# Optimization experiments

Measured on AMD Instinct MI355X. Metric: run time of the kernel, lower is better.

The kernel has to match this reference:

```python
import jax, jax.numpy as jnp
import numpy as np

B, SECL, WORDL, DIM = 16, 16, 256, 1024  # src_len = SECL*WORDL = 4096, dim = 2*hidden_dim
F_SIZE = 2  # config.mode == 'train'


def setup_inputs() -> dict:
    key = jax.random.key(0)
    ks = jax.random.split(key, 10)
    S = SECL * WORDL
    return {
        "dec_hidden": jax.random.normal(ks[0], (B, DIM), jnp.float32),
        "enc_output": jax.random.normal(ks[1], (B, S, DIM), jnp.float32),
        "enc_feature": jax.random.normal(ks[2], (B, S, DIM), jnp.float32),
        "enc_mask": jnp.ones((B, S), jnp.float32),
        "sec_attn": jax.random.uniform(ks[3], (B, SECL), jnp.float32),
        "coverage": jax.random.uniform(ks[4], (B, S), jnp.float32),
        "focus": jax.random.normal(ks[5], (B, SECL), jnp.float32),
        "W_dec": jax.random.normal(ks[6], (DIM, DIM), jnp.float32) * 0.02,
        "b_dec": jax.random.normal(ks[7], (DIM,), jnp.float32) * 0.02,
        "v": jax.random.normal(ks[8], (DIM,), jnp.float32) * 0.02,
        "w_cov": jax.random.normal(ks[9], (DIM,), jnp.float32) * 0.02,
    }


def reference(dec_hidden, enc_output, enc_feature, enc_mask, sec_attn, coverage, focus,
              W_dec, b_dec, v, w_cov):
    batch, src_len, dim = enc_output.shape
    secL = sec_attn.shape[1]
    wordL = src_len // secL

    # decode_proj(dec_hidden), broadcast over src_len; coverage feature = coverage * w_cov
    dec_feature = dec_hidden @ W_dec.T + b_dec                     # [B, D]
    att_features = (enc_feature + dec_feature[:, None, :]
                    + coverage[:, :, None] * w_cov[None, None, :])  # [B, S, D]
    score = jnp.einsum('bsd,d->bs', jnp.tanh(att_features), v)      # [B, S]

    # hard focus path: top-k sections, gather scores/mask, softmax, scatter back
    score3 = score.reshape(batch, secL, wordL)
    topk_focus, top_idx = jax.lax.top_k(focus, F_SIZE)              # [B, k]
    bidx = jnp.arange(batch)[:, None]
    score_g = score3[bidx, top_idx].reshape(batch, -1)              # [B, k*wordL]
    mask_g = enc_mask.reshape(batch, secL, wordL)[bidx, top_idx].reshape(batch, -1)

    attn_foc = jax.nn.softmax(score_g, axis=1) * mask_g
    attn_foc = attn_foc / attn_foc.sum(1, keepdims=True)
    attn_foc = topk_focus[:, :, None] * attn_foc.reshape(batch, F_SIZE, wordL)

    attn_full = jnp.zeros((batch, secL, wordL), score.dtype).at[bidx, top_idx, :].set(attn_foc)
    attn_dist = attn_full.reshape(batch, src_len)
    attn_dist = attn_dist / attn_dist.sum(1, keepdims=True)

    context = jnp.einsum('bs,bsd->bd', attn_dist, enc_output)       # [B, D]
    coverage_out = coverage + attn_dist                              # [B, S]
    return context, attn_dist, coverage_out
```

## Files before the change

kernel.cpp:

```cpp
#include <hip/hip_runtime.h>
#include <math.h>

#define BB      16
#define SECL    16
#define WORDL   256
#define SRCLEN  4096
#define DIM     1024
#define FSZ     2
#define GL      (FSZ*WORDL)

__device__ __forceinline__ float fast_tanh(float x) {
    x = fminf(fmaxf(x, -10.f), 10.f);
    float e = __expf(2.f * x);
    return 1.f - 2.f * __builtin_amdgcn_rcpf(e + 1.f);
}

__global__ __launch_bounds__(256) void k_decproj_topk(
    const float* __restrict__ dec_hidden, const float* __restrict__ W_dec,
    const float* __restrict__ b_dec, const float* __restrict__ focus,
    float* __restrict__ dec_feature, int* __restrict__ top_idx,
    float* __restrict__ top_val, float* __restrict__ context)
{
    if (blockIdx.x == 16) {
        int b = blockIdx.y;
        float4 z = {0.f, 0.f, 0.f, 0.f};
        ((float4*)(context + (size_t)b * DIM))[threadIdx.x] = z;
        if (threadIdx.x == 0) {
            const float* f = focus + b * SECL;
            int i0 = 0; float v0 = f[0];
            for (int s = 1; s < SECL; s++) if (f[s] > v0) { v0 = f[s]; i0 = s; }
            int i1 = -1; float v1 = -INFINITY;
            for (int s = 0; s < SECL; s++)
                if (s != i0 && f[s] > v1) { v1 = f[s]; i1 = s; }
            top_idx[b*2+0] = i0; top_idx[b*2+1] = i1;
            top_val[b*2+0] = v0; top_val[b*2+1] = v1;
        }
        return;
    }
    int b = blockIdx.y;
    int t = threadIdx.x;
    int i = blockIdx.x * 64 + (t >> 2);
    int c = t & 3;
    const float4* Wr = (const float4*)(W_dec + (size_t)i * DIM + c * 256);
    const float4* Dr = (const float4*)(dec_hidden + (size_t)b * DIM + c * 256);
    float acc = 0.f;
    #pragma unroll 8
    for (int j = 0; j < 64; j++) {
        float4 w = Wr[j], d = Dr[j];
        acc += w.x*d.x + w.y*d.y + w.z*d.z + w.w*d.w;
    }
    acc += __shfl_down(acc, 2);
    acc += __shfl_down(acc, 1);
    if (c == 0) dec_feature[(size_t)b * DIM + i] = acc + b_dec[i];
}

__global__ __launch_bounds__(256) void k_score_cov(
    const float* __restrict__ enc_feature, const float* __restrict__ coverage,
    const float* __restrict__ dec_feature, const float* __restrict__ v,
    const float* __restrict__ w_cov, const int* __restrict__ top_idx,
    float* __restrict__ score_g, float* __restrict__ cov_out)
{
    int bid = blockIdx.x;
    if (bid >= 2048) {
        int idx = (bid - 2048) * 256 + threadIdx.x;
        ((float4*)cov_out)[idx] = ((const float4*)coverage)[idx];
        return;
    }
    int w    = bid * 4 + (threadIdx.x >> 6);
    int lane = threadIdx.x & 63;
    int b  = w >> 9;
    int r  = w & 511;
    int k  = r >> 8;
    int wp = r & 255;
    int sec = top_idx[b*2 + k];
    int s   = sec * WORDL + wp;
    float cv = coverage[(size_t)b * SRCLEN + s];
    const float4* ef = (const float4*)(enc_feature + ((size_t)b * SRCLEN + s) * DIM);
    const float4* df = (const float4*)(dec_feature + (size_t)b * DIM);
    const float4* vv = (const float4*)v;
    const float4* wc = (const float4*)w_cov;
    float acc = 0.f;
    #pragma unroll
    for (int q = 0; q < 4; q++) {
        int e4 = q * 64 + lane;
        float4 a = ef[e4], d = df[e4], wcv = wc[e4], vt = vv[e4];
        acc += fast_tanh(a.x + d.x + cv * wcv.x) * vt.x;
        acc += fast_tanh(a.y + d.y + cv * wcv.y) * vt.y;
        acc += fast_tanh(a.z + d.z + cv * wcv.z) * vt.z;
        acc += fast_tanh(a.w + d.w + cv * wcv.w) * vt.w;
    }
    #pragma unroll
    for (int off = 32; off; off >>= 1) acc += __shfl_down(acc, off);
    if (lane == 0) score_g[b * GL + r] = acc;
}

__device__ __forceinline__ float block_reduce(float val, int is_max) {
    __shared__ float red[4];
    int lane = threadIdx.x & 63, wid = threadIdx.x >> 6;
    #pragma unroll
    for (int off = 32; off; off >>= 1) {
        float o = __shfl_down(val, off);
        val = is_max ? fmaxf(val, o) : val + o;
    }
    if (lane == 0) red[wid] = val;
    __syncthreads();
    if (threadIdx.x == 0) {
        float r = red[0];
        for (int i = 1; i < 4; i++) r = is_max ? fmaxf(r, red[i]) : r + red[i];
        red[0] = r;
    }
    __syncthreads();
    float result = red[0];
    __syncthreads();
    return result;
}

__global__ __launch_bounds__(256) void k_softmax_scatter(
    const float* __restrict__ enc_mask, const float* __restrict__ coverage,
    const int* __restrict__ top_idx, const float* __restrict__ top_val,
    const float* __restrict__ score_g,
    float* __restrict__ attn_g, float* __restrict__ attn_out,
    float* __restrict__ cov_out)
{
    int b = blockIdx.x;
    int t = threadIdx.x;

    float4 z = {0.f, 0.f, 0.f, 0.f};
    float4* arow = (float4*)(attn_out + (size_t)b * SRCLEN);
    #pragma unroll
    for (int u = 0; u < 4; u++) arow[t + u * 256] = z;

    float sc[2], mk[2], fv[2];
    int ss[2];
    #pragma unroll
    for (int u = 0; u < 2; u++) {
        int r  = t + u * 256;
        int k  = r >> 8, wp = r & 255;
        int sec = top_idx[b*2 + k];
        int s   = sec * WORDL + wp;
        ss[u] = s;
        sc[u] = score_g[b * GL + r];
        mk[u] = enc_mask[(size_t)b * SRCLEN + s];
        fv[u] = top_val[b*2 + k];
    }
    float m  = block_reduce(fmaxf(sc[0], sc[1]), 1);
    float e0 = __expf(sc[0] - m), e1 = __expf(sc[1] - m);
    float Tn = block_reduce(fv[0]*e0*mk[0] + fv[1]*e1*mk[1], 0);
    float inv = 1.0f / Tn;
    __syncthreads();
    #pragma unroll
    for (int u = 0; u < 2; u++) {
        int r = t + u * 256;
        float a = fv[u] * (u ? e1 : e0) * mk[u] * inv;
        attn_g[b * GL + r] = a;
        attn_out[(size_t)b * SRCLEN + ss[u]] = a;
        cov_out [(size_t)b * SRCLEN + ss[u]] = coverage[(size_t)b * SRCLEN + ss[u]] + a;
    }
}

__global__ __launch_bounds__(256) void k_context(
    const float* __restrict__ enc_output, const int* __restrict__ top_idx,
    const float* __restrict__ attn_g, float* __restrict__ context)
{
    int b  = blockIdx.y;
    int sp = blockIdx.x;
    int t  = threadIdx.x;
    int i0 = top_idx[b*2], i1 = top_idx[b*2 + 1];
    float4 acc = {0.f, 0.f, 0.f, 0.f};
    #pragma unroll 4
    for (int j = 0; j < 32; j++) {
        int r  = sp * 32 + j;
        int k  = r >> 8, wp = r & 255;
        int s  = (k ? i1 : i0) * WORDL + wp;
        float a = attn_g[b * GL + r];
        float4 e = ((const float4*)(enc_output + ((size_t)b * SRCLEN + s) * DIM))[t];
        acc.x += a * e.x; acc.y += a * e.y; acc.z += a * e.z; acc.w += a * e.w;
    }
    float* ctx = context + (size_t)b * DIM + t * 4;
    atomicAdd(ctx + 0, acc.x);
    atomicAdd(ctx + 1, acc.y);
    atomicAdd(ctx + 2, acc.z);
    atomicAdd(ctx + 3, acc.w);
}

extern "C" void kernel_launch(void* const* d_in, const int* in_sizes, int n_in,
                              void* d_out, int out_size, void* d_ws, size_t ws_size,
                              hipStream_t stream) {
    const float* dec_hidden  = (const float*)d_in[0];
    const float* enc_output  = (const float*)d_in[1];
    const float* enc_feature = (const float*)d_in[2];
    const float* enc_mask    = (const float*)d_in[3];
    const float* coverage    = (const float*)d_in[5];
    const float* focus       = (const float*)d_in[6];
    const float* W_dec       = (const float*)d_in[7];
    const float* b_dec       = (const float*)d_in[8];
    const float* v           = (const float*)d_in[9];
    const float* w_cov       = (const float*)d_in[10];

    float* out      = (float*)d_out;
    float* context  = out;
    float* attn_out = out + 16384;
    float* cov_out  = out + 16384 + 65536;

    float* ws          = (float*)d_ws;
    float* dec_feature = ws;
    int*   top_idx     = (int*)(ws + 16384);
    float* top_val     = ws + 16384 + 32;
    float* score_g     = ws + 16448;
    float* attn_g      = ws + 24640;

    k_decproj_topk<<<dim3(17, 16), 256, 0, stream>>>(
        dec_hidden, W_dec, b_dec, focus, dec_feature, top_idx, top_val, context);

    k_score_cov<<<dim3(2112), 256, 0, stream>>>(
        enc_feature, coverage, dec_feature, v, w_cov, top_idx, score_g, cov_out);

    k_softmax_scatter<<<dim3(16), 256, 0, stream>>>(
        enc_mask, coverage, top_idx, top_val, score_g, attn_g, attn_out, cov_out);

    k_context<<<dim3(16, 16), 256, 0, stream>>>(
        enc_output, top_idx, attn_g, context);
}
```

Measured before the change: 458.4 us.

## Recompute top-2 per wave, fuse coverage update into context kernel, drop workspace

The serial single-thread top-2 over focus is replaced by a wave-level shuffle reduction. Each kernel recomputes it locally, so the top_idx and top_val buffers go away. The separate coverage copy plus scattered coverage writes become one vectorised coverage+attn pass in an extra block of the context kernel. That kernel now reads attention weights straight from attn_out. Intermediates (dec_feature, score_g) are aliased into output buffers instead of workspace, which relies on the kernel order to avoid overwriting live data.

```diff
diff --git a/kernel.cpp b/kernel.cpp
--- a/kernel.cpp
+++ b/kernel.cpp
@@ -9,32 +9,46 @@
 #define FSZ     2
 #define GL      (FSZ*WORDL)
 
+
 __device__ __forceinline__ float fast_tanh(float x) {
     x = fminf(fmaxf(x, -10.f), 10.f);
     float e = __expf(2.f * x);
     return 1.f - 2.f * __builtin_amdgcn_rcpf(e + 1.f);
 }
 
-__global__ __launch_bounds__(256) void k_decproj_topk(
+__device__ __forceinline__ void wave_top2(const float* __restrict__ f, int lane,
+                                          int& i0_, float& v0_, int& i1_, float& v1_)
+{
+    int idx = lane & 15;
+    float x = f[idx];
+    float m = x; int mi = idx;
+    #pragma unroll
+    for (int off = 8; off; off >>= 1) {
+        float om = __shfl_xor(m, off);
+        int   oi = __shfl_xor(mi, off);
+        if (om > m || (om == m && oi < mi)) { m = om; mi = oi; }
+    }
+    i0_ = mi; v0_ = m;
+    float x2 = (idx == mi) ? -INFINITY : x;
+    float m2 = x2; int mi2 = idx;
+    #pragma unroll
+    for (int off = 8; off; off >>= 1) {
+        float om = __shfl_xor(m2, off);
+        int   oi = __shfl_xor(mi2, off);
+        if (om > m2 || (om == m2 && oi < mi2)) { m2 = om; mi2 = oi; }
+    }
+    i1_ = mi2; v1_ = m2;
+}
+
+__global__ __launch_bounds__(256) void k_decproj(
     const float* __restrict__ dec_hidden, const float* __restrict__ W_dec,
-    const float* __restrict__ b_dec, const float* __restrict__ focus,
-    float* __restrict__ dec_feature, int* __restrict__ top_idx,
-    float* __restrict__ top_val, float* __restrict__ context)
+    const float* __restrict__ b_dec,
+    float* __restrict__ dec_feature, float* __restrict__ context)
 {
     if (blockIdx.x == 16) {
         int b = blockIdx.y;
         float4 z = {0.f, 0.f, 0.f, 0.f};
         ((float4*)(context + (size_t)b * DIM))[threadIdx.x] = z;
-        if (threadIdx.x == 0) {
-            const float* f = focus + b * SECL;
-            int i0 = 0; float v0 = f[0];
-            for (int s = 1; s < SECL; s++) if (f[s] > v0) { v0 = f[s]; i0 = s; }
-            int i1 = -1; float v1 = -INFINITY;
-            for (int s = 0; s < SECL; s++)
-                if (s != i0 && f[s] > v1) { v1 = f[s]; i1 = s; }
-            top_idx[b*2+0] = i0; top_idx[b*2+1] = i1;
-            top_val[b*2+0] = v0; top_val[b*2+1] = v1;
-        }
         return;
     }
     int b = blockIdx.y;
@@ -54,26 +68,24 @@
     if (c == 0) dec_feature[(size_t)b * DIM + i] = acc + b_dec[i];
 }
 
-__global__ __launch_bounds__(256) void k_score_cov(
+__global__ __launch_bounds__(256) void k_score(
     const float* __restrict__ enc_feature, const float* __restrict__ coverage,
     const float* __restrict__ dec_feature, const float* __restrict__ v,
-    const float* __restrict__ w_cov, const int* __restrict__ top_idx,
-    float* __restrict__ score_g, float* __restrict__ cov_out)
-{
-    int bid = blockIdx.x;
-    if (bid >= 2048) {
-        int idx = (bid - 2048) * 256 + threadIdx.x;
-        ((float4*)cov_out)[idx] = ((const float4*)coverage)[idx];
-        return;
-    }
-    int w    = bid * 4 + (threadIdx.x >> 6);
+    const float* __restrict__ w_cov, const float* __restrict__ focus,
+    float* __restrict__ score_g)
+{
+    int w    = blockIdx.x * 4 + (threadIdx.x >> 6);
     int lane = threadIdx.x & 63;
     int b  = w >> 9;
     int r  = w & 511;
     int k  = r >> 8;
     int wp = r & 255;
-    int sec = top_idx[b*2 + k];
+
+    int i0, i1; float v0, v1;
+    wave_top2(focus + b * SECL, lane, i0, v0, i1, v1);
+    int sec = k ? i1 : i0;
     int s   = sec * WORDL + wp;
+
     float cv = coverage[(size_t)b * SRCLEN + s];
     const float4* ef = (const float4*)(enc_feature + ((size_t)b * SRCLEN + s) * DIM);
     const float4* df = (const float4*)(dec_feature + (size_t)b * DIM);
@@ -116,14 +128,15 @@
 }
 
 __global__ __launch_bounds__(256) void k_softmax_scatter(
-    const float* __restrict__ enc_mask, const float* __restrict__ coverage,
-    const int* __restrict__ top_idx, const float* __restrict__ top_val,
-    const float* __restrict__ score_g,
-    float* __restrict__ attn_g, float* __restrict__ attn_out,
-    float* __restrict__ cov_out)
+    const float* __restrict__ enc_mask, const float* __restrict__ focus,
+    const float* __restrict__ score_g, float* __restrict__ attn_out)
 {
     int b = blockIdx.x;
     int t = threadIdx.x;
+    int lane = t & 63;
+
+    int i0, i1; float v0, v1;
+    wave_top2(focus + b * SECL, lane, i0, v0, i1, v1);
 
     float4 z = {0.f, 0.f, 0.f, 0.f};
     float4* arow = (float4*)(attn_out + (size_t)b * SRCLEN);
@@ -136,12 +149,12 @@
     for (int u = 0; u < 2; u++) {
         int r  = t + u * 256;
         int k  = r >> 8, wp = r & 255;
-        int sec = top_idx[b*2 + k];
+        int sec = k ? i1 : i0;
         int s   = sec * WORDL + wp;
         ss[u] = s;
         sc[u] = score_g[b * GL + r];
         mk[u] = enc_mask[(size_t)b * SRCLEN + s];
-        fv[u] = top_val[b*2 + k];
+        fv[u] = k ? v1 : v0;
     }
     float m  = block_reduce(fmaxf(sc[0], sc[1]), 1);
     float e0 = __expf(sc[0] - m), e1 = __expf(sc[1] - m);
@@ -152,27 +165,44 @@
     for (int u = 0; u < 2; u++) {
         int r = t + u * 256;
         float a = fv[u] * (u ? e1 : e0) * mk[u] * inv;
-        attn_g[b * GL + r] = a;
         attn_out[(size_t)b * SRCLEN + ss[u]] = a;
-        cov_out [(size_t)b * SRCLEN + ss[u]] = coverage[(size_t)b * SRCLEN + ss[u]] + a;
-    }
-}
-
-__global__ __launch_bounds__(256) void k_context(
-    const float* __restrict__ enc_output, const int* __restrict__ top_idx,
-    const float* __restrict__ attn_g, float* __restrict__ context)
+    }
+}
+
+__global__ __launch_bounds__(256) void k_context_cov(
+    const float* __restrict__ enc_output, const float* __restrict__ coverage,
+    const float* __restrict__ focus, const float* __restrict__ attn_out,
+    float* __restrict__ context, float* __restrict__ cov_out)
 {
     int b  = blockIdx.y;
     int sp = blockIdx.x;
     int t  = threadIdx.x;
-    int i0 = top_idx[b*2], i1 = top_idx[b*2 + 1];
+
+    if (sp == 16) {
+        const float4* cv = (const float4*)(coverage + (size_t)b * SRCLEN);
+        const float4* at = (const float4*)(attn_out + (size_t)b * SRCLEN);
+        float4*       co = (float4*)(cov_out + (size_t)b * SRCLEN);
+        #pragma unroll
+        for (int u = 0; u < 4; u++) {
+            int j = t + u * 256;
+            float4 c = cv[j], a = at[j];
+            c.x += a.x; c.y += a.y; c.z += a.z; c.w += a.w;
+            co[j] = c;
+        }
+        return;
+    }
+
+    int lane = t & 63;
+    int i0, i1; float v0, v1;
+    wave_top2(focus + b * SECL, lane, i0, v0, i1, v1);
+
     float4 acc = {0.f, 0.f, 0.f, 0.f};
     #pragma unroll 4
     for (int j = 0; j < 32; j++) {
         int r  = sp * 32 + j;
         int k  = r >> 8, wp = r & 255;
         int s  = (k ? i1 : i0) * WORDL + wp;
-        float a = attn_g[b * GL + r];
+        float a = attn_out[(size_t)b * SRCLEN + s];
         float4 e = ((const float4*)(enc_output + ((size_t)b * SRCLEN + s) * DIM))[t];
         acc.x += a * e.x; acc.y += a * e.y; acc.z += a * e.z; acc.w += a * e.w;
     }
@@ -202,22 +232,19 @@
     float* attn_out = out + 16384;
     float* cov_out  = out + 16384 + 65536;
 
-    float* ws          = (float*)d_ws;
-    float* dec_feature = ws;
-    int*   top_idx     = (int*)(ws + 16384);
-    float* top_val     = ws + 16384 + 32;
-    float* score_g     = ws + 16448;
-    float* attn_g      = ws + 24640;
-
-    k_decproj_topk<<<dim3(17, 16), 256, 0, stream>>>(
-        dec_hidden, W_dec, b_dec, focus, dec_feature, top_idx, top_val, context);
-
-    k_score_cov<<<dim3(2112), 256, 0, stream>>>(
-        enc_feature, coverage, dec_feature, v, w_cov, top_idx, score_g, cov_out);
+    float* dec_feature = attn_out;
+    float* score_g     = cov_out;
+    (void)d_ws; (void)ws_size;
+
+    k_decproj<<<dim3(17, 16), 256, 0, stream>>>(
+        dec_hidden, W_dec, b_dec, dec_feature, context);
+
+    k_score<<<dim3(2048), 256, 0, stream>>>(
+        enc_feature, coverage, dec_feature, v, w_cov, focus, score_g);
 
     k_softmax_scatter<<<dim3(16), 256, 0, stream>>>(
-        enc_mask, coverage, top_idx, top_val, score_g, attn_g, attn_out, cov_out);
-
-    k_context<<<dim3(16, 16), 256, 0, stream>>>(
-        enc_output, top_idx, attn_g, context);
-}
+        enc_mask, focus, score_g, attn_out);
+
+    k_context_cov<<<dim3(17, 16), 256, 0, stream>>>(
+        enc_output, coverage, focus, attn_out, context, cov_out);
+}
```

Result: no change. 464.0 us (+1.2%).
